# Kernel optimization log

Hardware: AMD Instinct MI355X
Metric: run time of the kernel (lower is better)

The kernel has to match this reference:

```python
import jax, jax.numpy as jnp
import numpy as np

B, T, I, H, O = 1024, 512, 1, 64, 1


def _lstm_layer(x, Wih, Whh, bih, bhh):
    # x: [B,T,in]; Wih: [4H,in]; Whh: [4H,H]; biases: [4H]
    # Precompute input contribution for all timesteps (PyTorch adds both biases).
    xg = jnp.einsum('bti,gi->btg', x, Wih) + bih + bhh  # [B,T,4H]
    h0 = jnp.zeros((x.shape[0], H), x.dtype)

    def step(carry, xg_t):
        h, c = carry
        gates = xg_t + h @ Whh.T  # [B,4H], torch gate order i,f,g,o
        i, f, g, o = jnp.split(gates, 4, axis=-1)
        c = jax.nn.sigmoid(f) * c + jax.nn.sigmoid(i) * jnp.tanh(g)
        h = jax.nn.sigmoid(o) * jnp.tanh(c)
        return (h, c), h

    (_, _), hs = jax.lax.scan(step, (h0, h0), jnp.swapaxes(xg, 0, 1))
    return jnp.swapaxes(hs, 0, 1)  # [B,T,H]


def setup_inputs() -> dict:
    key = jax.random.key(0)
    ks = jax.random.split(key, 12)
    s = 1.0 / np.sqrt(H)  # torch LSTM/Linear init scale
    u = lambda k, shp: jax.random.uniform(k, shp, jnp.float32, -s, s)
    return {
        'x': jax.random.normal(ks[0], (B, T, I), jnp.float32),
        'W_ih0': u(ks[1], (4 * H, I)), 'W_hh0': u(ks[2], (4 * H, H)),
        'b_ih0': u(ks[3], (4 * H,)), 'b_hh0': u(ks[4], (4 * H,)),
        'W_ih1': u(ks[5], (4 * H, H)), 'W_hh1': u(ks[6], (4 * H, H)),
        'b_ih1': u(ks[7], (4 * H,)), 'b_hh1': u(ks[8], (4 * H,)),
        'W_fc': u(ks[9], (O, H)), 'b_fc': u(ks[10], (O,)),
    }


def reference(x, W_ih0, W_hh0, b_ih0, b_hh0, W_ih1, W_hh1, b_ih1, b_hh1, W_fc, b_fc):
    h1 = _lstm_layer(x, W_ih0, W_hh0, b_ih0, b_hh0)   # layer 0
    h2 = _lstm_layer(h1, W_ih1, W_hh1, b_ih1, b_hh1)  # layer 1
    return h2[:, -1, :] @ W_fc.T + b_fc  # [B,O]
```

## Files before the change

kernel.cpp:

```cpp
#include <hip/hip_runtime.h>

#define BB 1024
#define TT 512
#define HH 64
#define NB 4
#define NTHR 512

typedef _Float16 half8 __attribute__((ext_vector_type(8)));
typedef float f32x4 __attribute__((ext_vector_type(4)));

#if defined(__has_builtin)
#  if __has_builtin(__builtin_amdgcn_rcpf)
#    define FRCP(v) __builtin_amdgcn_rcpf(v)
#  endif
#endif
#ifndef FRCP
#  define FRCP(v) (1.0f / (v))
#endif

#define MFMA16(A, B, C) __builtin_amdgcn_mfma_f32_16x16x32_f16((A), (B), (C), 0, 0, 0)

__device__ __forceinline__ float fsig(float v) {
    return FRCP(1.0f + __expf(-v));
}
__device__ __forceinline__ float ftanh(float v) {
    return fmaf(2.0f, fsig(2.0f * v), -1.0f);
}

__device__ __forceinline__ half8 load_frag(const float* __restrict__ W, int row, int k0) {
    const float4* p = (const float4*)(W + row * HH + k0);
    float4 u = p[0], v = p[1];
    half8 r;
    r[0] = (_Float16)u.x; r[1] = (_Float16)u.y; r[2] = (_Float16)u.z; r[3] = (_Float16)u.w;
    r[4] = (_Float16)v.x; r[5] = (_Float16)v.y; r[6] = (_Float16)v.z; r[7] = (_Float16)v.w;
    return r;
}

__global__ __launch_bounds__(NTHR, 2)
void lstm_mfma7(const float* __restrict__ x,
                const float* __restrict__ Wih0,
                const float* __restrict__ Whh0,
                const float* __restrict__ bih0,
                const float* __restrict__ bhh0,
                const float* __restrict__ Wih1,
                const float* __restrict__ Whh1,
                const float* __restrict__ bih1,
                const float* __restrict__ bhh1,
                const float* __restrict__ Wfc,
                const float* __restrict__ bfc,
                float* __restrict__ out)
{
    __shared__ float s_x[NB][TT + 1];
    __shared__ __align__(16) _Float16 s_h0b[2][NB][80];
    __shared__ __align__(16) _Float16 s_h1b[2][NB][80];

    const int t    = threadIdx.x;
    const int lane = t & 63;
    const int w    = t >> 6;
    const int b0   = blockIdx.x * NB;

    const int arow = lane & 15;
    const int g4   = lane >> 4;
    const int bsrc = lane & 3;
    const int rep   = (lane >> 2) & 3;
    const int layer = rep & 1;
    const int dd    = rep >> 1;
    const int u     = 8 * w + 4 * dd + g4;

    half8 a0[2][2], a1i[2][2], a1h[2][2];
#pragma unroll
    for (int d = 0; d < 2; ++d) {
        const int row = (arow & 3) * 64 + 8 * w + 4 * d + (arow >> 2);
#pragma unroll
        for (int kk = 0; kk < 2; ++kk) {
            const int k0 = kk * 32 + g4 * 8;
            a0[d][kk]  = load_frag(Whh0, row, k0);
            a1i[d][kk] = load_frag(Wih1, row, k0);
            a1h[d][kk] = load_frag(Whh1, row, k0);
        }
    }

    f32x4 cb0[2], cb1[2];
#pragma unroll
    for (int d = 0; d < 2; ++d) {
        const int uu = 8 * w + 4 * d + g4;
#pragma unroll
        for (int q = 0; q < 4; ++q) {
            const int r = q * 64 + uu;
            cb0[d][q] = bih0[r] + bhh0[r];
            cb1[d][q] = bih1[r] + bhh1[r];
        }
    }
    float xw[4];
#pragma unroll
    for (int q = 0; q < 4; ++q) {
        xw[q] = (layer == 0) ? Wih0[q * 64 + u] : 0.0f;
    }

#pragma unroll
    for (int k = 0; k < (NB * TT) / NTHR; ++k) {
        int idx = t + NTHR * k;
        int nb  = idx >> 9;
        int pos = idx & (TT - 1);
        s_x[nb][pos] = x[(b0 + nb) * TT + pos];
    }
    {
        _Float16* z0 = &s_h0b[0][0][0];
        _Float16* z1 = &s_h1b[0][0][0];
        for (int i = t; i < 2 * NB * 80; i += NTHR) {
            z0[i] = (_Float16)0.0f;
            z1[i] = (_Float16)0.0f;
        }
    }

    float cst = 0.0f;
    const float* xp = &s_x[bsrc][0];
    __syncthreads();

#define STEP(RB, L0, L1, XS)                                                  \
    {                                                                         \
        const float xv = xp[XS];                                              \
        const _Float16* h0p = &s_h0b[RB][bsrc][g4 * 8];                       \
        const _Float16* h1p = &s_h1b[RB][bsrc][g4 * 8];                       \
        half8 bh0_0 = *(const half8*)(h0p);                                   \
        half8 bh0_1 = *(const half8*)(h0p + 32);                              \
        half8 bh1_0 = *(const half8*)(h1p);                                   \
        half8 bh1_1 = *(const half8*)(h1p + 32);                              \
        f32x4 c0_0 = cb0[0], c0_1 = cb0[1];                                   \
        c0_0 = MFMA16(a0[0][0], bh0_0, c0_0);                                 \
        c0_1 = MFMA16(a0[1][0], bh0_0, c0_1);                                 \
        c0_0 = MFMA16(a0[0][1], bh0_1, c0_0);                                 \
        c0_1 = MFMA16(a0[1][1], bh0_1, c0_1);                                 \
        f32x4 c1a0 = cb1[0], c1a1 = cb1[1];                                   \
        f32x4 c1b0 = {0.f, 0.f, 0.f, 0.f}, c1b1 = {0.f, 0.f, 0.f, 0.f};       \
        c1a0 = MFMA16(a1i[0][0], bh0_0, c1a0);                                \
        c1a1 = MFMA16(a1i[1][0], bh0_0, c1a1);                                \
        c1b0 = MFMA16(a1h[0][0], bh1_0, c1b0);                                \
        c1b1 = MFMA16(a1h[1][0], bh1_0, c1b1);                                \
        c1a0 = MFMA16(a1i[0][1], bh0_1, c1a0);                                \
        c1a1 = MFMA16(a1i[1][1], bh0_1, c1a1);                                \
        c1b0 = MFMA16(a1h[0][1], bh1_1, c1b0);                                \
        c1b1 = MFMA16(a1h[1][1], bh1_1, c1b1);                                \
        f32x4 c1_0 = c1a0 + c1b0;                                             \
        f32x4 c1_1 = c1a1 + c1b1;                                             \
        f32x4 t0 = dd ? c0_1 : c0_0;                                          \
        f32x4 t1 = dd ? c1_1 : c1_0;                                          \
        f32x4 gv = layer ? t1 : t0;                                           \
        float gi = fmaf(xw[0], xv, gv[0]);                                    \
        float gf = fmaf(xw[1], xv, gv[1]);                                    \
        float gg = fmaf(xw[2], xv, gv[2]);                                    \
        float go = fmaf(xw[3], xv, gv[3]);                                    \
        if ((L0) && (L1)) {                                                   \
            float i_ = fsig(gi);                                              \
            float f_ = fsig(gf);                                              \
            float g_ = ftanh(gg);                                             \
            float o_ = fsig(go);                                              \
            cst = fmaf(f_, cst, i_ * g_);                                     \
            float hn = o_ * ftanh(cst);                                       \
            _Float16* dst = layer ? &s_h1b[RB ^ 1][bsrc][u]                   \
                                  : &s_h0b[RB ^ 1][bsrc][u];                  \
            *dst = (_Float16)hn;                                              \
        } else if (L0) {                                                      \
            if (layer == 0) {                                                 \
                float i_ = fsig(gi);                                          \
                float f_ = fsig(gf);                                          \
                float g_ = ftanh(gg);                                         \
                float o_ = fsig(go);                                          \
                cst = fmaf(f_, cst, i_ * g_);                                 \
                s_h0b[RB ^ 1][bsrc][u] = (_Float16)(o_ * ftanh(cst));         \
            }                                                                 \
        } else {                                                              \
            if (layer == 1) {                                                 \
                float i_ = fsig(gi);                                          \
                float f_ = fsig(gf);                                          \
                float g_ = ftanh(gg);                                         \
                float o_ = fsig(go);                                          \
                cst = fmaf(f_, cst, i_ * g_);                                 \
                s_h1b[RB ^ 1][bsrc][u] = (_Float16)(o_ * ftanh(cst));         \
            }                                                                 \
        }                                                                     \
        __syncthreads();                                                      \
    }

    STEP(0, 1, 0, 0)
    {
        int s = 1;
#pragma nounroll
        for (int it = 0; it < (TT - 2) / 2; ++it) {
            STEP(1, 1, 1, s)
            STEP(0, 1, 1, s + 1)
            s += 2;
        }
    }
    STEP(1, 1, 1, 511)
    STEP(0, 0, 1, 511)
#undef STEP

    if (t < NB * HH) {
        const int nb = t >> 6;
        const int j  = t & 63;
        float v = (float)s_h1b[1][nb][j] * Wfc[j];
#pragma unroll
        for (int off = 32; off > 0; off >>= 1) {
            v += __shfl_down(v, off);
        }
        if (j == 0) out[b0 + nb] = v + bfc[0];
    }
}

extern "C" void kernel_launch(void* const* d_in, const int* in_sizes, int n_in,
                              void* d_out, int out_size, void* d_ws, size_t ws_size,
                              hipStream_t stream) {
    const float* x    = (const float*)d_in[0];
    const float* Wih0 = (const float*)d_in[1];
    const float* Whh0 = (const float*)d_in[2];
    const float* bih0 = (const float*)d_in[3];
    const float* bhh0 = (const float*)d_in[4];
    const float* Wih1 = (const float*)d_in[5];
    const float* Whh1 = (const float*)d_in[6];
    const float* bih1 = (const float*)d_in[7];
    const float* bhh1 = (const float*)d_in[8];
    const float* Wfc  = (const float*)d_in[9];
    const float* bfc  = (const float*)d_in[10];
    float* out = (float*)d_out;

    lstm_mfma7<<<dim3(BB / NB), dim3(NTHR), 0, stream>>>(
        x, Wih0, Whh0, bih0, bhh0, Wih1, Whh1, bih1, bhh1, Wfc, bfc, out);
}
```

Baseline: 294.2 us.

## Fold exp2 scaling into weights and read x directly from global memory

Pre-scales the weights and biases by -log2(e), or -2·log2(e) for the g gate, so each activation becomes a bare exp2 plus a reciprocal, with no multiply before the exponential. The tanh(c) output is rewritten as a single fma. The shared-memory staging of x is removed and x is now loaded from global memory inside the loop, two timesteps per iteration. This shortens the serial per-step activation chain, but it adds global-load latency inside the recurrent loop and folds the scale into the fp16 weights before rounding.

```diff
diff --git a/kernel.cpp b/kernel.cpp
--- a/kernel.cpp
+++ b/kernel.cpp
@@ -13,31 +13,46 @@
 #  if __has_builtin(__builtin_amdgcn_rcpf)
 #    define FRCP(v) __builtin_amdgcn_rcpf(v)
 #  endif
+#  if __has_builtin(__builtin_amdgcn_exp2f)
+#    define FEXP2(v) __builtin_amdgcn_exp2f(v)
+#  endif
 #endif
 #ifndef FRCP
 #  define FRCP(v) (1.0f / (v))
 #endif
+#ifndef FEXP2
+#  define FEXP2(v) exp2f(v)
+#endif
 
 #define MFMA16(A, B, C) __builtin_amdgcn_mfma_f32_16x16x32_f16((A), (B), (C), 0, 0, 0)
 
-__device__ __forceinline__ float fsig(float v) {
-    return FRCP(1.0f + __expf(-v));
-}
-__device__ __forceinline__ float ftanh(float v) {
-    return fmaf(2.0f, fsig(2.0f * v), -1.0f);
-}
-
-__device__ __forceinline__ half8 load_frag(const float* __restrict__ W, int row, int k0) {
+#define L2E 1.4426950408889634f
+
+__device__ __forceinline__ float lstm_act(float gi, float gf, float gg, float go,
+                                          float& cst) {
+    float i_ = FRCP(1.0f + FEXP2(gi));
+    float f_ = FRCP(1.0f + FEXP2(gf));
+    float o_ = FRCP(1.0f + FEXP2(go));
+    float g_ = fmaf(2.0f, FRCP(1.0f + FEXP2(gg)), -1.0f);
+    cst = fmaf(f_, cst, i_ * g_);
+    float e2 = FEXP2(cst * (-2.0f * L2E));
+    return fmaf(2.0f * o_, FRCP(1.0f + e2), -o_);
+}
+
+__device__ __forceinline__ half8 load_frag(const float* __restrict__ W, int row,
+                                           int k0, float sc) {
     const float4* p = (const float4*)(W + row * HH + k0);
     float4 u = p[0], v = p[1];
     half8 r;
-    r[0] = (_Float16)u.x; r[1] = (_Float16)u.y; r[2] = (_Float16)u.z; r[3] = (_Float16)u.w;
-    r[4] = (_Float16)v.x; r[5] = (_Float16)v.y; r[6] = (_Float16)v.z; r[7] = (_Float16)v.w;
+    r[0] = (_Float16)(u.x * sc); r[1] = (_Float16)(u.y * sc);
+    r[2] = (_Float16)(u.z * sc); r[3] = (_Float16)(u.w * sc);
+    r[4] = (_Float16)(v.x * sc); r[5] = (_Float16)(v.y * sc);
+    r[6] = (_Float16)(v.z * sc); r[7] = (_Float16)(v.w * sc);
     return r;
 }
 
 __global__ __launch_bounds__(NTHR, 2)
-void lstm_mfma7(const float* __restrict__ x,
+void lstm_mfma9(const float* __restrict__ x,
                 const float* __restrict__ Wih0,
                 const float* __restrict__ Whh0,
                 const float* __restrict__ bih0,
@@ -50,7 +65,6 @@
                 const float* __restrict__ bfc,
                 float* __restrict__ out)
 {
-    __shared__ float s_x[NB][TT + 1];
     __shared__ __align__(16) _Float16 s_h0b[2][NB][80];
     __shared__ __align__(16) _Float16 s_h1b[2][NB][80];
 
@@ -67,16 +81,19 @@
     const int dd    = rep >> 1;
     const int u     = 8 * w + 4 * dd + g4;
 
+    const int   gq  = arow & 3;
+    const float fsc = (gq == 2) ? (-2.0f * L2E) : (-L2E);
+
     half8 a0[2][2], a1i[2][2], a1h[2][2];
 #pragma unroll
     for (int d = 0; d < 2; ++d) {
-        const int row = (arow & 3) * 64 + 8 * w + 4 * d + (arow >> 2);
+        const int row = gq * 64 + 8 * w + 4 * d + (arow >> 2);
 #pragma unroll
         for (int kk = 0; kk < 2; ++kk) {
             const int k0 = kk * 32 + g4 * 8;
-            a0[d][kk]  = load_frag(Whh0, row, k0);
-            a1i[d][kk] = load_frag(Wih1, row, k0);
-            a1h[d][kk] = load_frag(Whh1, row, k0);
+            a0[d][kk]  = load_frag(Whh0, row, k0, fsc);
+            a1i[d][kk] = load_frag(Wih1, row, k0, fsc);
+            a1h[d][kk] = load_frag(Whh1, row, k0, fsc);
         }
     }
 
@@ -87,23 +104,20 @@
 #pragma unroll
         for (int q = 0; q < 4; ++q) {
             const int r = q * 64 + uu;
-            cb0[d][q] = bih0[r] + bhh0[r];
-            cb1[d][q] = bih1[r] + bhh1[r];
+            const float sq = (q == 2) ? (-2.0f * L2E) : (-L2E);
+            cb0[d][q] = (bih0[r] + bhh0[r]) * sq;
+            cb1[d][q] = (bih1[r] + bhh1[r]) * sq;
         }
     }
     float xw[4];
 #pragma unroll
     for (int q = 0; q < 4; ++q) {
-        xw[q] = (layer == 0) ? Wih0[q * 64 + u] : 0.0f;
-    }
-
-#pragma unroll
-    for (int k = 0; k < (NB * TT) / NTHR; ++k) {
-        int idx = t + NTHR * k;
-        int nb  = idx >> 9;
-        int pos = idx & (TT - 1);
-        s_x[nb][pos] = x[(b0 + nb) * TT + pos];
-    }
+        const float sq = (q == 2) ? (-2.0f * L2E) : (-L2E);
+        xw[q] = (layer == 0) ? (Wih0[q * 64 + u] * sq) : 0.0f;
+    }
+
+    const float* __restrict__ xgp = x + (size_t)(b0 + bsrc) * TT;
+
     {
         _Float16* z0 = &s_h0b[0][0][0];
         _Float16* z1 = &s_h1b[0][0][0];
@@ -114,12 +128,10 @@
     }
 
     float cst = 0.0f;
-    const float* xp = &s_x[bsrc][0];
     __syncthreads();
 
-#define STEP(RB, L0, L1, XS)                                                  \
+#define STEP(RB, L0, L1, XV)                                                  \
     {                                                                         \
-        const float xv = xp[XS];                                              \
         const _Float16* h0p = &s_h0b[RB][bsrc][g4 * 8];                       \
         const _Float16* h1p = &s_h1b[RB][bsrc][g4 * 8];                       \
         half8 bh0_0 = *(const half8*)(h0p);                                   \
@@ -131,6 +143,7 @@
         c0_1 = MFMA16(a0[1][0], bh0_0, c0_1);                                 \
         c0_0 = MFMA16(a0[0][1], bh0_1, c0_0);                                 \
         c0_1 = MFMA16(a0[1][1], bh0_1, c0_1);                                 \
+             \
         f32x4 c1a0 = cb1[0], c1a1 = cb1[1];                                   \
         f32x4 c1b0 = {0.f, 0.f, 0.f, 0.f}, c1b1 = {0.f, 0.f, 0.f, 0.f};       \
         c1a0 = MFMA16(a1i[0][0], bh0_0, c1a0);                                \
@@ -146,54 +159,43 @@
         f32x4 t0 = dd ? c0_1 : c0_0;                                          \
         f32x4 t1 = dd ? c1_1 : c1_0;                                          \
         f32x4 gv = layer ? t1 : t0;                                           \
-        float gi = fmaf(xw[0], xv, gv[0]);                                    \
-        float gf = fmaf(xw[1], xv, gv[1]);                                    \
-        float gg = fmaf(xw[2], xv, gv[2]);                                    \
-        float go = fmaf(xw[3], xv, gv[3]);                                    \
+        float gi = fmaf(xw[0], (XV), gv[0]);                                  \
+        float gf = fmaf(xw[1], (XV), gv[1]);                                  \
+        float gg = fmaf(xw[2], (XV), gv[2]);                                  \
+        float go = fmaf(xw[3], (XV), gv[3]);                                  \
         if ((L0) && (L1)) {                                                   \
-            float i_ = fsig(gi);                                              \
-            float f_ = fsig(gf);                                              \
-            float g_ = ftanh(gg);                                             \
-            float o_ = fsig(go);                                              \
-            cst = fmaf(f_, cst, i_ * g_);                                     \
-            float hn = o_ * ftanh(cst);                                       \
+            float hn = lstm_act(gi, gf, gg, go, cst);                         \
             _Float16* dst = layer ? &s_h1b[RB ^ 1][bsrc][u]                   \
                                   : &s_h0b[RB ^ 1][bsrc][u];                  \
             *dst = (_Float16)hn;                                              \
         } else if (L0) {                                                      \
             if (layer == 0) {                                                 \
-                float i_ = fsig(gi);                                          \
-                float f_ = fsig(gf);                                          \
-                float g_ = ftanh(gg);                                         \
-                float o_ = fsig(go);                                          \
-                cst = fmaf(f_, cst, i_ * g_);                                 \
-                s_h0b[RB ^ 1][bsrc][u] = (_Float16)(o_ * ftanh(cst));         \
+                float hn = lstm_act(gi, gf, gg, go, cst);                     \
+                s_h0b[RB ^ 1][bsrc][u] = (_Float16)hn;                        \
             }                                                                 \
         } else {                                                              \
             if (layer == 1) {                                                 \
-                float i_ = fsig(gi);                                          \
-                float f_ = fsig(gf);                                          \
-                float g_ = ftanh(gg);                                         \
-                float o_ = fsig(go);                                          \
-                cst = fmaf(f_, cst, i_ * g_);                                 \
-                s_h1b[RB ^ 1][bsrc][u] = (_Float16)(o_ * ftanh(cst));         \
+                float hn = lstm_act(gi, gf, gg, go, cst);                     \
+                s_h1b[RB ^ 1][bsrc][u] = (_Float16)hn;                        \
             }                                                                 \
         }                                                                     \
         __syncthreads();                                                      \
     }
 
-    STEP(0, 1, 0, 0)
+    STEP(0, 1, 0, xgp[0])
     {
         int s = 1;
 #pragma nounroll
         for (int it = 0; it < (TT - 2) / 2; ++it) {
-            STEP(1, 1, 1, s)
-            STEP(0, 1, 1, s + 1)
+            const float xA = xgp[s];
+            const float xB = xgp[s + 1];
+            STEP(1, 1, 1, xA)
+            STEP(0, 1, 1, xB)
             s += 2;
         }
     }
-    STEP(1, 1, 1, 511)
-    STEP(0, 0, 1, 511)
+    STEP(1, 1, 1, xgp[511])
+    STEP(0, 0, 1, 0.0f)
 #undef STEP
 
     if (t < NB * HH) {
@@ -224,6 +226,6 @@
     const float* bfc  = (const float*)d_in[10];
     float* out = (float*)d_out;
 
-    lstm_mfma7<<<dim3(BB / NB), dim3(NTHR), 0, stream>>>(
+    lstm_mfma9<<<dim3(BB / NB), dim3(NTHR), 0, stream>>>(
         x, Wih0, Whh0, bih0, bhh0, Wih1, Whh1, bih1, bhh1, Wfc, bfc, out);
 }
```

Result: no change. 291.0 us (-1.1%).
